# Kernel tuning notes

Hardware: AMD Instinct MI355X
Metric: run time of the kernel (lower is better)

## Reference

```python
import jax, jax.numpy as jnp
import numpy as np

B, N, D, H = 2, 2048, 1024, 16
HD = D // H  # 64
EPS = 1e-6


def setup_inputs() -> dict:
    key = jax.random.key(0)
    ks = jax.random.split(key, 16)
    rnd = lambda k, shp: jax.random.normal(k, shp, dtype=jnp.float32)
    w = lambda k, i, o: rnd(k, (i, o)) * 0.02  # stored as (in, out); y = x @ W
    return {
        "x": rnd(ks[0], (B, N, D)),
        "emb_B_D": rnd(ks[1], (B, D)),
        "gate": rnd(ks[2], (B, D)),
        "crossattn_emb": rnd(ks[3], (B, 128, D)),
        "rope_emb_L_1_1_D": rnd(ks[4], (N, HD)),
        "Wq1": w(ks[5], D, D), "Wq2": w(ks[6], D, D),
        "Wk1": w(ks[7], D, D), "Wk2": w(ks[8], D, D),
        "Wv": w(ks[9], D, D),
        "Wo": w(ks[10], D, D),
        "Wada1": w(ks[11], D, D),
        "Wada2": w(ks[12], D, 2 * D),
        "bada2": jnp.zeros((2 * D,), dtype=jnp.float32),
    }


def rotate_half(t):
    t1, t2 = jnp.split(t, 2, axis=-1)
    return jnp.concatenate([-t2, t1], axis=-1)


def reference(x, emb_B_D, gate, crossattn_emb, rope_emb_L_1_1_D,
              Wq1, Wq2, Wk1, Wk2, Wv, Wo, Wada1, Wada2, bada2):
    # adaLN modulation: SiLU -> Linear(no bias) -> Linear(bias)
    ada = jax.nn.silu(emb_B_D) @ Wada1 @ Wada2 + bada2          # [B, 2D]
    shift, scale = jnp.split(ada, 2, axis=1)                    # [B, D] each

    # LayerNorm (no affine) + scale/shift
    mu = jnp.mean(x, axis=-1, keepdims=True)
    var = jnp.var(x, axis=-1, keepdims=True)
    xn = (x - mu) * jax.lax.rsqrt(var + EPS)
    xn = xn * (1.0 + scale[:, None, :]) + shift[:, None, :]     # [B, N, D]

    # QKV projections (each to_q/to_k is two stacked linears, to_v one)
    q = xn @ Wq1 @ Wq2
    k = xn @ Wk1 @ Wk2
    v = xn @ Wv
    split_heads = lambda t: t.reshape(B, N, H, HD).transpose(0, 2, 1, 3)  # b h n d
    q, k, v = split_heads(q), split_heads(k), split_heads(v)

    # RoPE
    cos = jnp.cos(rope_emb_L_1_1_D)[None, None]                 # [1,1,N,HD]
    sin = jnp.sin(rope_emb_L_1_1_D)[None, None]
    q = q * cos + rotate_half(q) * sin
    k = k * cos + rotate_half(k) * sin

    # Attention
    sim = jnp.einsum("bhid,bhjd->bhij", q, k) * (HD ** -0.5)
    attn = jax.nn.softmax(sim, axis=-1)
    out = jnp.einsum("bhij,bhjd->bhid", attn, v)
    out = out.transpose(0, 2, 1, 3).reshape(B, N, D) @ Wo

    # Gated residual
    return x + gate[:, None, :] * out
```

## Files before the change

### kernel.cpp

```cpp
#include <hip/hip_runtime.h>
#include <stdint.h>
#include <math.h>

typedef unsigned short u16;
typedef __attribute__((ext_vector_type(8))) short short8;
typedef __attribute__((ext_vector_type(4))) float f32x4;
typedef __attribute__((ext_vector_type(4))) unsigned short u16x4;
typedef __attribute__((ext_vector_type(2))) unsigned int uint2v;

#define DEV static __device__ __forceinline__

DEV u16 f2bf(float f) {
    unsigned u = __builtin_bit_cast(unsigned, f);
    u = u + 0x7fffu + ((u >> 16) & 1u);
    return (u16)(u >> 16);
}
DEV float bf2f(u16 s) { return __builtin_bit_cast(float, ((unsigned)s) << 16); }
DEV unsigned pk2(float a, float b) {
    unsigned ua = __builtin_bit_cast(unsigned, a) + 0x8000u;
    unsigned ub = __builtin_bit_cast(unsigned, b) + 0x8000u;
    return (ua >> 16) | (ub & 0xffff0000u);
}

DEV void gl_lds16(const u16* g, u16* l) {
#if __has_builtin(__builtin_amdgcn_global_load_lds)
    __builtin_amdgcn_global_load_lds((const __attribute__((address_space(1))) unsigned int*)g,
                                     (__attribute__((address_space(3))) unsigned int*)l, 16, 0, 0);
#else
    *(short8*)l = *(const short8*)g;
#endif
}


__global__ __launch_bounds__(256) void k_ada1(const float* __restrict__ emb, const float* __restrict__ W,
                                              float* __restrict__ out) {
    int col = blockIdx.x * 64 + (threadIdx.x & 63);
    int b = blockIdx.y;
    int kseg = threadIdx.x >> 6;
    float acc = 0.f;
    for (int k = kseg * 256; k < kseg * 256 + 256; k++) {
        float e = emb[b * 1024 + k];
        float se = e / (1.f + __expf(-e));
        acc += se * W[(size_t)k * 1024 + col];
    }
    __shared__ float red[4][64];
    red[kseg][threadIdx.x & 63] = acc;
    __syncthreads();
    if (threadIdx.x < 64)
        out[b * 1024 + blockIdx.x * 64 + threadIdx.x] =
            red[0][threadIdx.x] + red[1][threadIdx.x] + red[2][threadIdx.x] + red[3][threadIdx.x];
}

__global__ __launch_bounds__(256) void k_ada2(const float* __restrict__ t, const float* __restrict__ W,
                                              const float* __restrict__ bias, float* __restrict__ out) {
    int col = blockIdx.x * 64 + (threadIdx.x & 63);
    int b = blockIdx.y;
    int kseg = threadIdx.x >> 6;
    float acc = 0.f;
    for (int k = kseg * 256; k < kseg * 256 + 256; k++)
        acc += t[b * 1024 + k] * W[(size_t)k * 2048 + col];
    __shared__ float red[4][64];
    red[kseg][threadIdx.x & 63] = acc;
    __syncthreads();
    if (threadIdx.x < 64) {
        int c = blockIdx.x * 64 + threadIdx.x;
        out[b * 2048 + c] = red[0][threadIdx.x] + red[1][threadIdx.x] +
                            red[2][threadIdx.x] + red[3][threadIdx.x] + bias[c];
    }
}

__global__ __launch_bounds__(256) void k_conv(const float* s0, u16* d0, const float* s1, u16* d1,
                                              const float* s2, u16* d2, const float* s3, u16* d3,
                                              const float* s4, u16* d4, const float* s5, u16* d5) {
    __shared__ u16 tile[64][65];
    const float* s; u16* d;
    switch (blockIdx.z) {
        case 0: s = s0; d = d0; break;
        case 1: s = s1; d = d1; break;
        case 2: s = s2; d = d2; break;
        case 3: s = s3; d = d3; break;
        case 4: s = s4; d = d4; break;
        default: s = s5; d = d5; break;
    }
    int k0 = blockIdx.x * 64, n0 = blockIdx.y * 64;
    int tx = threadIdx.x & 63, ty = threadIdx.x >> 6;
    if (blockIdx.z >= 4) {
        #pragma unroll
        for (int i = 0; i < 16; i++) {
            int kk = ty + 4 * i;
            d[(size_t)(k0 + kk) * 1024 + n0 + tx] = f2bf(s[(size_t)(k0 + kk) * 1024 + n0 + tx]);
        }
        return;
    }
    #pragma unroll
    for (int i = 0; i < 16; i++) {
        int kk = ty + 4 * i;
        tile[kk][tx] = f2bf(s[(size_t)(k0 + kk) * 1024 + n0 + tx]);
    }
    __syncthreads();
    #pragma unroll
    for (int i = 0; i < 16; i++) {
        int nn = ty + 4 * i;
        d[(size_t)(n0 + nn) * 1024 + k0 + tx] = tile[tx][nn];
    }
}

__global__ __launch_bounds__(256) void k_ln(const float* __restrict__ x, const float* __restrict__ ada,
                                            u16* __restrict__ xn, const float* __restrict__ rope,
                                            float* __restrict__ cst, float* __restrict__ snt) {
    if (blockIdx.x < 512) {
        int idx = blockIdx.x * 256 + threadIdx.x;
        float sv, cv;
        __sincosf(rope[idx], &sv, &cv);
        cst[idx] = cv; snt[idx] = sv;
    }
    int row = blockIdx.x;
    int b = row >> 11;
    float4 v = ((const float4*)(x + (size_t)row * 1024))[threadIdx.x];
    float s = v.x + v.y + v.z + v.w;
    float ss = v.x * v.x + v.y * v.y + v.z * v.z + v.w * v.w;
    #pragma unroll
    for (int m = 1; m < 64; m <<= 1) { s += __shfl_xor(s, m, 64); ss += __shfl_xor(ss, m, 64); }
    __shared__ float red[2][4];
    int wave = threadIdx.x >> 6, lane = threadIdx.x & 63;
    if (lane == 0) { red[0][wave] = s; red[1][wave] = ss; }
    __syncthreads();
    s = red[0][0] + red[0][1] + red[0][2] + red[0][3];
    ss = red[1][0] + red[1][1] + red[1][2] + red[1][3];
    float mu = s * (1.f / 1024.f);
    float var = ss * (1.f / 1024.f) - mu * mu;
    float rs = rsqrtf(var + 1e-6f);
    int c = threadIdx.x * 4;
    const float* sh = ada + b * 2048;
    const float* sc = ada + b * 2048 + 1024;
    u16x4 r;
    r.x = f2bf((v.x - mu) * rs * (1.f + sc[c + 0]) + sh[c + 0]);
    r.y = f2bf((v.y - mu) * rs * (1.f + sc[c + 1]) + sh[c + 1]);
    r.z = f2bf((v.z - mu) * rs * (1.f + sc[c + 2]) + sh[c + 2]);
    r.w = f2bf((v.w - mu) * rs * (1.f + sc[c + 3]) + sh[c + 3]);
    *(u16x4*)(xn + (size_t)row * 1024 + c) = r;
}

template <int BM, int BN, int MODE>
DEV void gemm_core(const u16* __restrict__ A, const u16* __restrict__ Bt,
                   u16* __restrict__ Cb, float* __restrict__ Cf,
                   const float* __restrict__ Xres, const float* __restrict__ gate,
                   const float* __restrict__ cst, const float* __restrict__ snt,
                   float scale, int Nn, int K, int m0, int n0) {
    constexpr int MI = BM / 32, NJ = BN / 32;
    __shared__ u16 As[BM][64];
    __shared__ u16 Bs[BN][64];
    int tid = threadIdx.x;
    int lane = tid & 63, wave = tid >> 6;
    int wm = (wave & 1) * (BM / 2), wn = (wave >> 1) * (BN / 2);
    int lr = lane & 15, quad = lane >> 4;
    f32x4 acc[MI][NJ];
    #pragma unroll
    for (int i = 0; i < MI; i++)
        #pragma unroll
        for (int j = 0; j < NJ; j++) acc[i][j] = f32x4{0.f, 0.f, 0.f, 0.f};

    int arow = tid >> 3;
    int acol = (tid & 7) * 8;
    int g8 = (((tid & 7) ^ (arow & 7))) * 8;
    int cc[2] = { ((quad ^ (lr & 7))) * 8, (((4 + quad) ^ (lr & 7))) * 8 };

    for (int k0 = 0; k0 < K; k0 += 64) {
        #pragma unroll
        for (int p = 0; p < MI; p++)
            gl_lds16(A + (size_t)(m0 + arow + 32 * p) * K + k0 + g8, &As[arow + 32 * p][acol]);
        #pragma unroll
        for (int p = 0; p < NJ; p++)
            gl_lds16(Bt + (size_t)(n0 + arow + 32 * p) * K + k0 + g8, &Bs[arow + 32 * p][acol]);
        __syncthreads();
        #pragma unroll
        for (int ks = 0; ks < 2; ks++) {
            short8 af[MI], bfr[NJ];
            #pragma unroll
            for (int i = 0; i < MI; i++) af[i] = *(const short8*)(&As[wm + i * 16 + lr][cc[ks]]);
            #pragma unroll
            for (int j = 0; j < NJ; j++) bfr[j] = *(const short8*)(&Bs[wn + j * 16 + lr][cc[ks]]);
            #pragma unroll
            for (int i = 0; i < MI; i++)
                #pragma unroll
                for (int j = 0; j < NJ; j++)
                    acc[i][j] = __builtin_amdgcn_mfma_f32_16x16x32_bf16(af[i], bfr[j], acc[i][j], 0, 0, 0);
        }
        __syncthreads();
    }

    if (MODE == 2 && (n0 + wn) < 2048) {
        #pragma unroll
        for (int i = 0; i < MI; i++)
            #pragma unroll
            for (int jp = 0; jp < 2; jp++)
                #pragma unroll
                for (int r = 0; r < 4; r++) {
                    int row = m0 + wm + i * 16 + quad * 4 + r;
                    int n = row & 2047;
                    int d1 = jp * 16 + lr;
                    float c1 = cst[n * 64 + d1],      s1 = snt[n * 64 + d1];
                    float c2 = cst[n * 64 + d1 + 32], s2 = snt[n * 64 + d1 + 32];
                    float x1 = acc[i][jp][r], x2 = acc[i][jp + 2][r];
                    Cb[(size_t)row * Nn + n0 + wn + d1]      = f2bf(x1 * c1 - x2 * s1);
                    Cb[(size_t)row * Nn + n0 + wn + d1 + 32] = f2bf(x2 * c2 + x1 * s2);
                }
        return;
    }
    #pragma unroll
    for (int i = 0; i < MI; i++)
        #pragma unroll
        for (int j = 0; j < NJ; j++)
            #pragma unroll
            for (int r = 0; r < 4; r++) {
                int row = m0 + wm + i * 16 + quad * 4 + r;
                int col = n0 + wn + j * 16 + lr;
                float v = acc[i][j][r];
                if (MODE == 1) {
                    int b = row >> 11;
                    Cf[(size_t)row * Nn + col] = Xres[(size_t)row * Nn + col] + gate[b * 1024 + col] * v;
                } else {
                    Cb[(size_t)row * Nn + col] = f2bf(v * scale);
                }
            }
}

template <int BM, int BN, int MODE>
__global__ __launch_bounds__(256) void gemm_bt(const u16* __restrict__ A, const u16* __restrict__ Bt,
                                               u16* __restrict__ Cb, float* __restrict__ Cf,
                                               const float* __restrict__ Xres, const float* __restrict__ gate,
                                               const float* __restrict__ cst, const float* __restrict__ snt,
                                               int Nn, int K) {
    gemm_core<BM, BN, MODE>(A, Bt, Cb, Cf, Xres, gate, cst, snt, 1.f, Nn, K,
                            blockIdx.y * BM, blockIdx.x * BN);
}

__global__ __launch_bounds__(256) void gemm_fold(const u16* A0, const u16* B0, u16* C0,
                                                 const u16* A1, const u16* B1, u16* C1) {
    const u16* A = blockIdx.z ? A1 : A0;
    const u16* Bt = blockIdx.z ? B1 : B0;
    u16* C = blockIdx.z ? C1 : C0;
    float scale = blockIdx.z ? 1.0f : 0.125f;
    gemm_core<64, 64, 0>(A, Bt, C, nullptr, nullptr, nullptr, nullptr, nullptr, scale,
                         1024, 1024, blockIdx.y * 64, blockIdx.x * 64);
}

__global__ __launch_bounds__(256) void k_vtrans(const u16* __restrict__ v, u16* __restrict__ vt) {
    __shared__ u16 tile[64][65];
    int n0 = blockIdx.x * 64;
    int bh = blockIdx.y; int b = bh >> 4, h = bh & 15;
    int tx = threadIdx.x & 63, ty = threadIdx.x >> 6;
    #pragma unroll
    for (int i = 0; i < 16; i++) {
        int nn = ty + 4 * i;
        tile[nn][tx] = v[(size_t)(b * 2048 + n0 + nn) * 3072 + 2048 + h * 64 + tx];
    }
    __syncthreads();
    #pragma unroll
    for (int i = 0; i < 16; i++) {
        int dd = ty + 4 * i;
        vt[((size_t)bh * 64 + dd) * 2048 + n0 + tx] = tile[tx][dd];
    }
}

__global__ __launch_bounds__(256) void k_attn(const u16* __restrict__ qkv, const u16* __restrict__ vt,
                                              float* __restrict__ paO, float* __restrict__ paL) {
    __shared__ u16 pool[128 * 72];
    __shared__ u16 Ks[2][64][64];
    __shared__ u16 Vs[2][64][64];
    int q0 = blockIdx.x * 128;
    int bh = blockIdx.y; int b = bh >> 4, h = bh & 15;
    int z = blockIdx.z;
    int kbase = z * 1024;
    int tid = threadIdx.x;
    int lane = tid & 63, wave = tid >> 6;
    int lr = lane & 15, quad = lane >> 4;
    int srow = tid >> 3, scol = (tid & 7) * 8;
    int sg = (((tid & 7) ^ (srow & 7))) * 8;
    int cc[2] = { ((quad ^ (lr & 7))) * 8, (((4 + quad) ^ (lr & 7))) * 8 };

    const u16* kp = qkv + ((size_t)(b * 2048 + kbase + srow)) * 3072 + 1024 + h * 64 + sg;
    const u16* vp = vt + ((size_t)(bh * 64 + srow)) * 2048 + kbase + sg;

    #pragma unroll
    for (int p = 0; p < 4; p++)
        gl_lds16(qkv + ((size_t)(b * 2048 + q0 + srow + 32 * p)) * 3072 + h * 64 + sg,
                 pool + (srow + 32 * p) * 64 + scol);

    short8 krA[2], vrA[2], krB[2], vrB[2];
    krA[0] = *(const short8*)(kp);               krA[1] = *(const short8*)(kp + (size_t)32 * 3072);
    vrA[0] = *(const short8*)(vp);               vrA[1] = *(const short8*)(vp + (size_t)32 * 2048);
    __syncthreads();
    short8 qf[2][2];
    #pragma unroll
    for (int rt = 0; rt < 2; rt++)
        #pragma unroll
        for (int ks = 0; ks < 2; ks++)
            qf[rt][ks] = *(const short8*)(pool + (wave * 32 + rt * 16 + lr) * 64 + cc[ks]);
    *(short8*)(&Ks[0][srow][scol])      = krA[0];
    *(short8*)(&Ks[0][srow + 32][scol]) = krA[1];
    *(short8*)(&Vs[0][srow][scol])      = vrA[0];
    *(short8*)(&Vs[0][srow + 32][scol]) = vrA[1];
    krB[0] = *(const short8*)(kp + (size_t)64 * 3072);  krB[1] = *(const short8*)(kp + (size_t)96 * 3072);
    vrB[0] = *(const short8*)(vp + 64);                 vrB[1] = *(const short8*)(vp + 64 + (size_t)32 * 2048);
    __syncthreads();

    float l_part[2] = {0.f, 0.f};
    f32x4 oacc[2][4];
    #pragma unroll
    for (int rt = 0; rt < 2; rt++)
        #pragma unroll
        for (int dt = 0; dt < 4; dt++) oacc[rt][dt] = f32x4{0.f, 0.f, 0.f, 0.f};

    auto body = [&](int it, int cur, short8 (&krF)[2], short8 (&vrF)[2],
                    short8 (&krH)[2], short8 (&vrH)[2]) {
        if (it < 14) {
            const u16* kq = kp + (size_t)(it + 2) * 64 * 3072;
            const u16* vq = vp + (it + 2) * 64;
            krF[0] = *(const short8*)(kq);  krF[1] = *(const short8*)(kq + (size_t)32 * 3072);
            vrF[0] = *(const short8*)(vq);  vrF[1] = *(const short8*)(vq + (size_t)32 * 2048);
        }
        f32x4 st[2][4];
        #pragma unroll
        for (int rt = 0; rt < 2; rt++)
            #pragma unroll
            for (int ct = 0; ct < 4; ct++) st[rt][ct] = f32x4{0.f, 0.f, 0.f, 0.f};
        #pragma unroll
        for (int ks = 0; ks < 2; ks++) {
            short8 kf[4];
            #pragma unroll
            for (int ct = 0; ct < 4; ct++)
                kf[ct] = *(const short8*)(&Ks[cur][ct * 16 + lr][cc[ks]]);
            #pragma unroll
            for (int rt = 0; rt < 2; rt++)
                #pragma unroll
                for (int ct = 0; ct < 4; ct++)
                    st[rt][ct] = __builtin_amdgcn_mfma_f32_16x16x32_bf16(kf[ct], qf[rt][ks], st[rt][ct], 0, 0, 0);
        }
        #pragma unroll
        for (int rt = 0; rt < 2; rt++)
            #pragma unroll
            for (int ct = 0; ct < 4; ct++) {
                float p0 = __expf(st[rt][ct][0]);
                float p1 = __expf(st[rt][ct][1]);
                float p2 = __expf(st[rt][ct][2]);
                float p3 = __expf(st[rt][ct][3]);
                l_part[rt] += (p0 + p1) + (p2 + p3);
                uint2v w; w.x = pk2(p0, p1); w.y = pk2(p2, p3);
                *(uint2v*)(pool + (wave * 32 + rt * 16 + lr) * 72 + ct * 16 + quad * 4) = w;
            }
        #pragma unroll
        for (int ks = 0; ks < 2; ks++) {
            short8 pf[2], vf[4];
            #pragma unroll
            for (int rt = 0; rt < 2; rt++)
                pf[rt] = *(const short8*)(pool + (wave * 32 + rt * 16 + lr) * 72 + ks * 32 + quad * 8);
            #pragma unroll
            for (int dt = 0; dt < 4; dt++)
                vf[dt] = *(const short8*)(&Vs[cur][dt * 16 + lr][cc[ks]]);
            #pragma unroll
            for (int rt = 0; rt < 2; rt++)
                #pragma unroll
                for (int dt = 0; dt < 4; dt++)
                    oacc[rt][dt] = __builtin_amdgcn_mfma_f32_16x16x32_bf16(pf[rt], vf[dt], oacc[rt][dt], 0, 0, 0);
        }
        if (it < 15) {
            int nxt = cur ^ 1;
            *(short8*)(&Ks[nxt][srow][scol])      = krH[0];
            *(short8*)(&Ks[nxt][srow + 32][scol]) = krH[1];
            *(short8*)(&Vs[nxt][srow][scol])      = vrH[0];
            *(short8*)(&Vs[nxt][srow + 32][scol]) = vrH[1];
        }
        __syncthreads();
    };

    #pragma unroll 1
    for (int it2 = 0; it2 < 8; ++it2) {
        body(2 * it2,     0, krA, vrA, krB, vrB);
        body(2 * it2 + 1, 1, krB, vrB, krA, vrA);
    }

    #pragma unroll
    for (int rt = 0; rt < 2; rt++) {
        float l = l_part[rt];
        l += __shfl_xor(l, 16, 64);
        l += __shfl_xor(l, 32, 64);
        if (quad == 0)
            paL[(size_t)z * 65536 + bh * 2048 + q0 + wave * 32 + rt * 16 + lr] = l;
    }
    float* po = paO + (size_t)z * 4096 * 1024;
    #pragma unroll
    for (int rt = 0; rt < 2; rt++)
        #pragma unroll
        for (int dt = 0; dt < 4; dt++)
            #pragma unroll
            for (int r = 0; r < 4; r++) {
                int row = q0 + wave * 32 + rt * 16 + quad * 4 + r;
                po[((size_t)(b * 2048 + row)) * 1024 + h * 64 + dt * 16 + lr] = oacc[rt][dt][r];
            }
}

__global__ __launch_bounds__(256) void k_comb(const float* __restrict__ paO, const float* __restrict__ paL,
                                              u16* __restrict__ aob) {
    int row = blockIdx.x;
    int b = row >> 11, n = row & 2047;
    int c = threadIdx.x * 4;
    int h = c >> 6;
    float l0 = paL[(b * 16 + h) * 2048 + n];
    float l1 = paL[65536 + (b * 16 + h) * 2048 + n];
    float inv = 1.f / (l0 + l1);
    float4 o0 = *(const float4*)(paO + (size_t)row * 1024 + c);
    float4 o1 = *(const float4*)(paO + (size_t)4096 * 1024 + (size_t)row * 1024 + c);
    u16x4 r;
    r.x = f2bf((o0.x + o1.x) * inv);
    r.y = f2bf((o0.y + o1.y) * inv);
    r.z = f2bf((o0.z + o1.z) * inv);
    r.w = f2bf((o0.w + o1.w) * inv);
    *(u16x4*)(aob + (size_t)row * 1024 + c) = r;
}

extern "C" void kernel_launch(void* const* d_in, const int* in_sizes, int n_in,
                              void* d_out, int out_size, void* d_ws, size_t ws_size,
                              hipStream_t stream) {
    const float* x     = (const float*)d_in[0];
    const float* emb   = (const float*)d_in[1];
    const float* gate  = (const float*)d_in[2];
    const float* rope  = (const float*)d_in[4];
    const float* Wq1   = (const float*)d_in[5];
    const float* Wq2   = (const float*)d_in[6];
    const float* Wk1   = (const float*)d_in[7];
    const float* Wk2   = (const float*)d_in[8];
    const float* Wv    = (const float*)d_in[9];
    const float* Wo    = (const float*)d_in[10];
    const float* Wada1 = (const float*)d_in[11];
    const float* Wada2 = (const float*)d_in[12];
    const float* bada2 = (const float*)d_in[13];
    float* out = (float*)d_out;

    char* ws = (char*)d_ws;
    size_t off = 0;
    auto alloc = [&](size_t bytes) { void* p = ws + off; off += (bytes + 255) & ~(size_t)255; return p; };
    float* t_ada = (float*)alloc(2048 * 4);
    float* ada   = (float*)alloc(4096 * 4);
    float* cst   = (float*)alloc((size_t)131072 * 4);
    float* snt   = (float*)alloc((size_t)131072 * 4);
    u16* xn    = (u16*)alloc((size_t)4096 * 1024 * 2);
    u16* Wq1b  = (u16*)alloc((size_t)1024 * 1024 * 2);
    u16* Wk1b  = (u16*)alloc((size_t)1024 * 1024 * 2);
    u16* Wq2t  = (u16*)alloc((size_t)1024 * 1024 * 2);
    u16* Wk2t  = (u16*)alloc((size_t)1024 * 1024 * 2);
    u16* Wot   = (u16*)alloc((size_t)1024 * 1024 * 2);
    u16* WqkvT = (u16*)alloc((size_t)3072 * 1024 * 2);
    u16* qkvb  = (u16*)alloc((size_t)4096 * 3072 * 2);
    u16* vtb   = (u16*)alloc((size_t)4096 * 1024 * 2);
    u16* aob   = (u16*)alloc((size_t)4096 * 1024 * 2);
    float* paO = (float*)alloc((size_t)2 * 4096 * 1024 * 4);
    float* paL = (float*)alloc((size_t)2 * 65536 * 4);
    (void)ws_size; (void)in_sizes; (void)n_in; (void)out_size;

    k_ada1<<<dim3(16, 2), 256, 0, stream>>>(emb, Wada1, t_ada);
    k_ada2<<<dim3(32, 2), 256, 0, stream>>>(t_ada, Wada2, bada2, ada);

    k_conv<<<dim3(16, 16, 6), 256, 0, stream>>>(Wq2, Wq2t, Wk2, Wk2t,
                                                Wv, WqkvT + (size_t)2048 * 1024, Wo, Wot,
                                                Wq1, Wq1b, Wk1, Wk1b);

    k_ln<<<4096, 256, 0, stream>>>(x, ada, xn, rope, cst, snt);

    gemm_fold<<<dim3(16, 16, 2), 256, 0, stream>>>(Wq2t, Wq1b, WqkvT,
                                                   Wk2t, Wk1b, WqkvT + (size_t)1024 * 1024);

    gemm_bt<128, 128, 2><<<dim3(24, 32), 256, 0, stream>>>(xn, WqkvT, qkvb, nullptr, nullptr, nullptr,
                                                           cst, snt, 3072, 1024);

    k_vtrans<<<dim3(32, 32), 256, 0, stream>>>(qkvb, vtb);

    k_attn<<<dim3(16, 32, 2), 256, 0, stream>>>(qkvb, vtb, paO, paL);
    k_comb<<<4096, 256, 0, stream>>>(paO, paL, aob);

    gemm_bt<128, 64, 1><<<dim3(16, 32), 256, 0, stream>>>(aob, Wot, nullptr, out, x, gate,
                                                          nullptr, nullptr, 1024, 1024);
}
```

Baseline: 306.5 us.

## Fuse prep kernels, write V transposed from QKV GEMM, bf16 attention partials

Merges the ada2 linear and the RoPE sin/cos table into the weight-conversion kernel, so k_ada2 no longer runs as its own launch and the table leaves k_ln. The QKV GEMM epilogue now writes V directly in transposed per-head layout, which removes the k_vtrans kernel and shrinks the qkv buffer to Q and K only. Attention partial outputs are stored as bf16 in a thread-local dump layout instead of fp32 rows, cutting split-combine traffic. Softmax uses hardware exp2 with log2(e) folded into the Q scale. Storing partials in bf16 loses some precision before normalization.

```diff
diff --git a/kernel.cpp b/kernel.cpp
--- a/kernel.cpp
+++ b/kernel.cpp
@@ -20,6 +20,13 @@
     unsigned ua = __builtin_bit_cast(unsigned, a) + 0x8000u;
     unsigned ub = __builtin_bit_cast(unsigned, b) + 0x8000u;
     return (ua >> 16) | (ub & 0xffff0000u);
+}
+DEV float fexp2(float x) {
+#if __has_builtin(__builtin_amdgcn_exp2f)
+    return __builtin_amdgcn_exp2f(x);
+#else
+    return __expf(x * 0.69314718056f);
+#endif
 }
 
 DEV void gl_lds16(const u16* g, u16* l) {
@@ -51,28 +58,44 @@
             red[0][threadIdx.x] + red[1][threadIdx.x] + red[2][threadIdx.x] + red[3][threadIdx.x];
 }
 
-__global__ __launch_bounds__(256) void k_ada2(const float* __restrict__ t, const float* __restrict__ W,
-                                              const float* __restrict__ bias, float* __restrict__ out) {
-    int col = blockIdx.x * 64 + (threadIdx.x & 63);
-    int b = blockIdx.y;
-    int kseg = threadIdx.x >> 6;
-    float acc = 0.f;
-    for (int k = kseg * 256; k < kseg * 256 + 256; k++)
-        acc += t[b * 1024 + k] * W[(size_t)k * 2048 + col];
+__global__ __launch_bounds__(256) void k_prep(const float* s0, u16* d0, const float* s1, u16* d1,
+                                              const float* s2, u16* d2, const float* s3, u16* d3,
+                                              const float* s4, u16* d4, const float* s5, u16* d5,
+                                              const float* __restrict__ t_ada, const float* __restrict__ Wada2,
+                                              const float* __restrict__ bada2, float* __restrict__ ada,
+                                              const float* __restrict__ rope,
+                                              float* __restrict__ cst, float* __restrict__ snt) {
+    __shared__ u16 tile[64][65];
     __shared__ float red[4][64];
-    red[kseg][threadIdx.x & 63] = acc;
-    __syncthreads();
-    if (threadIdx.x < 64) {
-        int c = blockIdx.x * 64 + threadIdx.x;
-        out[b * 2048 + c] = red[0][threadIdx.x] + red[1][threadIdx.x] +
-                            red[2][threadIdx.x] + red[3][threadIdx.x] + bias[c];
-    }
-}
-
-__global__ __launch_bounds__(256) void k_conv(const float* s0, u16* d0, const float* s1, u16* d1,
-                                              const float* s2, u16* d2, const float* s3, u16* d3,
-                                              const float* s4, u16* d4, const float* s5, u16* d5) {
-    __shared__ u16 tile[64][65];
+    if (blockIdx.z == 6) {
+        int flat = blockIdx.y * 16 + blockIdx.x;
+        if (flat < 64) {
+            int b = flat >> 5, xb = flat & 31;
+            int col = xb * 64 + (threadIdx.x & 63);
+            int kseg = threadIdx.x >> 6;
+            float acc = 0.f;
+            for (int k = kseg * 256; k < kseg * 256 + 256; k++)
+                acc += t_ada[b * 1024 + k] * Wada2[(size_t)k * 2048 + col];
+            red[kseg][threadIdx.x & 63] = acc;
+            __syncthreads();
+            if (threadIdx.x < 64) {
+                int c = xb * 64 + threadIdx.x;
+                ada[b * 2048 + c] = red[0][threadIdx.x] + red[1][threadIdx.x] +
+                                    red[2][threadIdx.x] + red[3][threadIdx.x] + bada2[c];
+            }
+        } else if (flat < 192) {
+            int idx = (flat - 64) * 1024 + threadIdx.x * 4;
+            float4 rv = *(const float4*)(rope + idx);
+            float4 cv, sv;
+            __sincosf(rv.x, &sv.x, &cv.x);
+            __sincosf(rv.y, &sv.y, &cv.y);
+            __sincosf(rv.z, &sv.z, &cv.z);
+            __sincosf(rv.w, &sv.w, &cv.w);
+            *(float4*)(cst + idx) = cv;
+            *(float4*)(snt + idx) = sv;
+        }
+        return;
+    }
     const float* s; u16* d;
     switch (blockIdx.z) {
         case 0: s = s0; d = d0; break;
@@ -106,14 +129,7 @@
 }
 
 __global__ __launch_bounds__(256) void k_ln(const float* __restrict__ x, const float* __restrict__ ada,
-                                            u16* __restrict__ xn, const float* __restrict__ rope,
-                                            float* __restrict__ cst, float* __restrict__ snt) {
-    if (blockIdx.x < 512) {
-        int idx = blockIdx.x * 256 + threadIdx.x;
-        float sv, cv;
-        __sincosf(rope[idx], &sv, &cv);
-        cst[idx] = cv; snt[idx] = sv;
-    }
+                                            u16* __restrict__ xn) {
     int row = blockIdx.x;
     int b = row >> 11;
     float4 v = ((const float4*)(x + (size_t)row * 1024))[threadIdx.x];
@@ -143,7 +159,7 @@
 
 template <int BM, int BN, int MODE>
 DEV void gemm_core(const u16* __restrict__ A, const u16* __restrict__ Bt,
-                   u16* __restrict__ Cb, float* __restrict__ Cf,
+                   u16* __restrict__ Cb, float* __restrict__ Cf, u16* __restrict__ Vt,
                    const float* __restrict__ Xres, const float* __restrict__ gate,
                    const float* __restrict__ cst, const float* __restrict__ snt,
                    float scale, int Nn, int K, int m0, int n0) {
@@ -189,22 +205,38 @@
         __syncthreads();
     }
 
-    if (MODE == 2 && (n0 + wn) < 2048) {
-        #pragma unroll
-        for (int i = 0; i < MI; i++)
-            #pragma unroll
-            for (int jp = 0; jp < 2; jp++)
+    if (MODE == 2) {
+        if ((n0 + wn) < 2048) {
+            #pragma unroll
+            for (int i = 0; i < MI; i++)
                 #pragma unroll
-                for (int r = 0; r < 4; r++) {
-                    int row = m0 + wm + i * 16 + quad * 4 + r;
-                    int n = row & 2047;
-                    int d1 = jp * 16 + lr;
-                    float c1 = cst[n * 64 + d1],      s1 = snt[n * 64 + d1];
-                    float c2 = cst[n * 64 + d1 + 32], s2 = snt[n * 64 + d1 + 32];
-                    float x1 = acc[i][jp][r], x2 = acc[i][jp + 2][r];
-                    Cb[(size_t)row * Nn + n0 + wn + d1]      = f2bf(x1 * c1 - x2 * s1);
-                    Cb[(size_t)row * Nn + n0 + wn + d1 + 32] = f2bf(x2 * c2 + x1 * s2);
+                for (int jp = 0; jp < 2; jp++)
+                    #pragma unroll
+                    for (int r = 0; r < 4; r++) {
+                        int row = m0 + wm + i * 16 + quad * 4 + r;
+                        int n = row & 2047;
+                        int d1 = jp * 16 + lr;
+                        float c1 = cst[n * 64 + d1],      s1 = snt[n * 64 + d1];
+                        float c2 = cst[n * 64 + d1 + 32], s2 = snt[n * 64 + d1 + 32];
+                        float x1 = acc[i][jp][r], x2 = acc[i][jp + 2][r];
+                        Cb[(size_t)row * Nn + n0 + wn + d1]      = f2bf(x1 * c1 - x2 * s1);
+                        Cb[(size_t)row * Nn + n0 + wn + d1 + 32] = f2bf(x2 * c2 + x1 * s2);
+                    }
+        } else {
+            int hv = (n0 + wn - 2048) >> 6;
+            #pragma unroll
+            for (int i = 0; i < MI; i++)
+                #pragma unroll
+                for (int j = 0; j < NJ; j++) {
+                    int token = m0 + wm + i * 16 + quad * 4;
+                    int bb = token >> 11;
+                    int nloc = token & 2047;
+                    u16x4 w;
+                    w.x = f2bf(acc[i][j][0]); w.y = f2bf(acc[i][j][1]);
+                    w.z = f2bf(acc[i][j][2]); w.w = f2bf(acc[i][j][3]);
+                    *(u16x4*)(Vt + ((size_t)((bb * 16 + hv) * 64 + j * 16 + lr)) * 2048 + nloc) = w;
                 }
+        }
         return;
     }
     #pragma unroll
@@ -228,10 +260,11 @@
 template <int BM, int BN, int MODE>
 __global__ __launch_bounds__(256) void gemm_bt(const u16* __restrict__ A, const u16* __restrict__ Bt,
                                                u16* __restrict__ Cb, float* __restrict__ Cf,
+                                               u16* __restrict__ Vt,
                                                const float* __restrict__ Xres, const float* __restrict__ gate,
                                                const float* __restrict__ cst, const float* __restrict__ snt,
                                                int Nn, int K) {
-    gemm_core<BM, BN, MODE>(A, Bt, Cb, Cf, Xres, gate, cst, snt, 1.f, Nn, K,
+    gemm_core<BM, BN, MODE>(A, Bt, Cb, Cf, Vt, Xres, gate, cst, snt, 1.f, Nn, K,
                             blockIdx.y * BM, blockIdx.x * BN);
 }
 
@@ -240,31 +273,13 @@
     const u16* A = blockIdx.z ? A1 : A0;
     const u16* Bt = blockIdx.z ? B1 : B0;
     u16* C = blockIdx.z ? C1 : C0;
-    float scale = blockIdx.z ? 1.0f : 0.125f;
-    gemm_core<64, 64, 0>(A, Bt, C, nullptr, nullptr, nullptr, nullptr, nullptr, scale,
+    float scale = blockIdx.z ? 1.0f : 0.18033688f;
+    gemm_core<64, 64, 0>(A, Bt, C, nullptr, nullptr, nullptr, nullptr, nullptr, nullptr, scale,
                          1024, 1024, blockIdx.y * 64, blockIdx.x * 64);
 }
 
-__global__ __launch_bounds__(256) void k_vtrans(const u16* __restrict__ v, u16* __restrict__ vt) {
-    __shared__ u16 tile[64][65];
-    int n0 = blockIdx.x * 64;
-    int bh = blockIdx.y; int b = bh >> 4, h = bh & 15;
-    int tx = threadIdx.x & 63, ty = threadIdx.x >> 6;
-    #pragma unroll
-    for (int i = 0; i < 16; i++) {
-        int nn = ty + 4 * i;
-        tile[nn][tx] = v[(size_t)(b * 2048 + n0 + nn) * 3072 + 2048 + h * 64 + tx];
-    }
-    __syncthreads();
-    #pragma unroll
-    for (int i = 0; i < 16; i++) {
-        int dd = ty + 4 * i;
-        vt[((size_t)bh * 64 + dd) * 2048 + n0 + tx] = tile[tx][dd];
-    }
-}
-
 __global__ __launch_bounds__(256) void k_attn(const u16* __restrict__ qkv, const u16* __restrict__ vt,
-                                              float* __restrict__ paO, float* __restrict__ paL) {
+                                              u16* __restrict__ dump, float* __restrict__ paL) {
     __shared__ u16 pool[128 * 72];
     __shared__ u16 Ks[2][64][64];
     __shared__ u16 Vs[2][64][64];
@@ -279,16 +294,16 @@
     int sg = (((tid & 7) ^ (srow & 7))) * 8;
     int cc[2] = { ((quad ^ (lr & 7))) * 8, (((4 + quad) ^ (lr & 7))) * 8 };
 
-    const u16* kp = qkv + ((size_t)(b * 2048 + kbase + srow)) * 3072 + 1024 + h * 64 + sg;
+    const u16* kp = qkv + ((size_t)(b * 2048 + kbase + srow)) * 2048 + 1024 + h * 64 + sg;
     const u16* vp = vt + ((size_t)(bh * 64 + srow)) * 2048 + kbase + sg;
 
     #pragma unroll
     for (int p = 0; p < 4; p++)
-        gl_lds16(qkv + ((size_t)(b * 2048 + q0 + srow + 32 * p)) * 3072 + h * 64 + sg,
+        gl_lds16(qkv + ((size_t)(b * 2048 + q0 + srow + 32 * p)) * 2048 + h * 64 + sg,
                  pool + (srow + 32 * p) * 64 + scol);
 
     short8 krA[2], vrA[2], krB[2], vrB[2];
-    krA[0] = *(const short8*)(kp);               krA[1] = *(const short8*)(kp + (size_t)32 * 3072);
+    krA[0] = *(const short8*)(kp);               krA[1] = *(const short8*)(kp + (size_t)32 * 2048);
     vrA[0] = *(const short8*)(vp);               vrA[1] = *(const short8*)(vp + (size_t)32 * 2048);
     __syncthreads();
     short8 qf[2][2];
@@ -301,7 +316,7 @@
     *(short8*)(&Ks[0][srow + 32][scol]) = krA[1];
     *(short8*)(&Vs[0][srow][scol])      = vrA[0];
     *(short8*)(&Vs[0][srow + 32][scol]) = vrA[1];
-    krB[0] = *(const short8*)(kp + (size_t)64 * 3072);  krB[1] = *(const short8*)(kp + (size_t)96 * 3072);
+    krB[0] = *(const short8*)(kp + (size_t)64 * 2048);  krB[1] = *(const short8*)(kp + (size_t)96 * 2048);
     vrB[0] = *(const short8*)(vp + 64);                 vrB[1] = *(const short8*)(vp + 64 + (size_t)32 * 2048);
     __syncthreads();
 
@@ -315,9 +330,9 @@
     auto body = [&](int it, int cur, short8 (&krF)[2], short8 (&vrF)[2],
                     short8 (&krH)[2], short8 (&vrH)[2]) {
         if (it < 14) {
-            const u16* kq = kp + (size_t)(it + 2) * 64 * 3072;
+            const u16* kq = kp + (size_t)(it + 2) * 64 * 2048;
             const u16* vq = vp + (it + 2) * 64;
-            krF[0] = *(const short8*)(kq);  krF[1] = *(const short8*)(kq + (size_t)32 * 3072);
+            krF[0] = *(const short8*)(kq);  krF[1] = *(const short8*)(kq + (size_t)32 * 2048);
             vrF[0] = *(const short8*)(vq);  vrF[1] = *(const short8*)(vq + (size_t)32 * 2048);
         }
         f32x4 st[2][4];
@@ -341,10 +356,10 @@
         for (int rt = 0; rt < 2; rt++)
             #pragma unroll
             for (int ct = 0; ct < 4; ct++) {
-                float p0 = __expf(st[rt][ct][0]);
-                float p1 = __expf(st[rt][ct][1]);
-                float p2 = __expf(st[rt][ct][2]);
-                float p3 = __expf(st[rt][ct][3]);
+                float p0 = fexp2(st[rt][ct][0]);
+                float p1 = fexp2(st[rt][ct][1]);
+                float p2 = fexp2(st[rt][ct][2]);
+                float p3 = fexp2(st[rt][ct][3]);
                 l_part[rt] += (p0 + p1) + (p2 + p3);
                 uint2v w; w.x = pk2(p0, p1); w.y = pk2(p2, p3);
                 *(uint2v*)(pool + (wave * 32 + rt * 16 + lr) * 72 + ct * 16 + quad * 4) = w;
@@ -388,35 +403,50 @@
         if (quad == 0)
             paL[(size_t)z * 65536 + bh * 2048 + q0 + wave * 32 + rt * 16 + lr] = l;
     }
-    float* po = paO + (size_t)z * 4096 * 1024;
+    u16* dp = dump + (size_t)z * 4194304 + ((size_t)(bh * 16 + blockIdx.x) * 256 + tid) * 32;
     #pragma unroll
     for (int rt = 0; rt < 2; rt++)
         #pragma unroll
-        for (int dt = 0; dt < 4; dt++)
+        for (int dt = 0; dt < 4; dt++) {
+            u16x4 w;
+            w.x = f2bf(oacc[rt][dt][0]); w.y = f2bf(oacc[rt][dt][1]);
+            w.z = f2bf(oacc[rt][dt][2]); w.w = f2bf(oacc[rt][dt][3]);
+            *(u16x4*)(dp + rt * 16 + dt * 4) = w;
+        }
+}
+
+__global__ __launch_bounds__(256) void k_comb(const u16* __restrict__ dump, const float* __restrict__ paL,
+                                              u16* __restrict__ aob) {
+    int bx = blockIdx.x, bh = blockIdx.y;
+    int b = bh >> 4, h = bh & 15;
+    int tid = threadIdx.x;
+    int lane = tid & 63, wave = tid >> 6;
+    int lr = lane & 15, quad = lane >> 4;
+    int q0 = bx * 128;
+    const u16* d0 = dump + ((size_t)(bh * 16 + bx) * 256 + tid) * 32;
+    const u16* d1 = d0 + 4194304;
+    #pragma unroll
+    for (int rt = 0; rt < 2; rt++) {
+        float inv[4];
+        #pragma unroll
+        for (int r = 0; r < 4; r++) {
+            int row = q0 + wave * 32 + rt * 16 + quad * 4 + r;
+            float l0 = paL[bh * 2048 + row];
+            float l1 = paL[65536 + bh * 2048 + row];
+            inv[r] = 1.f / (l0 + l1);
+        }
+        #pragma unroll
+        for (int dt = 0; dt < 4; dt++) {
+            u16x4 w0 = *(const u16x4*)(d0 + rt * 16 + dt * 4);
+            u16x4 w1 = *(const u16x4*)(d1 + rt * 16 + dt * 4);
             #pragma unroll
             for (int r = 0; r < 4; r++) {
                 int row = q0 + wave * 32 + rt * 16 + quad * 4 + r;
-                po[((size_t)(b * 2048 + row)) * 1024 + h * 64 + dt * 16 + lr] = oacc[rt][dt][r];
+                float o = (bf2f(((const u16*)&w0)[r]) + bf2f(((const u16*)&w1)[r])) * inv[r];
+                aob[((size_t)(b * 2048 + row)) * 1024 + h * 64 + dt * 16 + lr] = f2bf(o);
             }
-}
-
-__global__ __launch_bounds__(256) void k_comb(const float* __restrict__ paO, const float* __restrict__ paL,
-                                              u16* __restrict__ aob) {
-    int row = blockIdx.x;
-    int b = row >> 11, n = row & 2047;
-    int c = threadIdx.x * 4;
-    int h = c >> 6;
-    float l0 = paL[(b * 16 + h) * 2048 + n];
-    float l1 = paL[65536 + (b * 16 + h) * 2048 + n];
-    float inv = 1.f / (l0 + l1);
-    float4 o0 = *(const float4*)(paO + (size_t)row * 1024 + c);
-    float4 o1 = *(const float4*)(paO + (size_t)4096 * 1024 + (size_t)row * 1024 + c);
-    u16x4 r;
-    r.x = f2bf((o0.x + o1.x) * inv);
-    r.y = f2bf((o0.y + o1.y) * inv);
-    r.z = f2bf((o0.z + o1.z) * inv);
-    r.w = f2bf((o0.w + o1.w) * inv);
-    *(u16x4*)(aob + (size_t)row * 1024 + c) = r;
+        }
+    }
 }
 
 extern "C" void kernel_launch(void* const* d_in, const int* in_sizes, int n_in,
@@ -451,33 +481,31 @@
     u16* Wk2t  = (u16*)alloc((size_t)1024 * 1024 * 2);
     u16* Wot   = (u16*)alloc((size_t)1024 * 1024 * 2);
     u16* WqkvT = (u16*)alloc((size_t)3072 * 1024 * 2);
-    u16* qkvb  = (u16*)alloc((size_t)4096 * 3072 * 2);
+    u16* qkvb  = (u16*)alloc((size_t)4096 * 2048 * 2);
     u16* vtb   = (u16*)alloc((size_t)4096 * 1024 * 2);
     u16* aob   = (u16*)alloc((size_t)4096 * 1024 * 2);
-    float* paO = (float*)alloc((size_t)2 * 4096 * 1024 * 4);
+    u16* dumpO = (u16*)alloc((size_t)2 * 4194304 * 2);
     float* paL = (float*)alloc((size_t)2 * 65536 * 4);
     (void)ws_size; (void)in_sizes; (void)n_in; (void)out_size;
 
     k_ada1<<<dim3(16, 2), 256, 0, stream>>>(emb, Wada1, t_ada);
-    k_ada2<<<dim3(32, 2), 256, 0, stream>>>(t_ada, Wada2, bada2, ada);
-
-    k_conv<<<dim3(16, 16, 6), 256, 0, stream>>>(Wq2, Wq2t, Wk2, Wk2t,
+
+    k_prep<<<dim3(16, 16, 7), 256, 0, stream>>>(Wq2, Wq2t, Wk2, Wk2t,
                                                 Wv, WqkvT + (size_t)2048 * 1024, Wo, Wot,
-                                                Wq1, Wq1b, Wk1, Wk1b);
-
-    k_ln<<<4096, 256, 0, stream>>>(x, ada, xn, rope, cst, snt);
+                                                Wq1, Wq1b, Wk1, Wk1b,
+                                                t_ada, Wada2, bada2, ada, rope, cst, snt);
+
+    k_ln<<<4096, 256, 0, stream>>>(x, ada, xn);
 
     gemm_fold<<<dim3(16, 16, 2), 256, 0, stream>>>(Wq2t, Wq1b, WqkvT,
                                                    Wk2t, Wk1b, WqkvT + (size_t)1024 * 1024);
 
-    gemm_bt<128, 128, 2><<<dim3(24, 32), 256, 0, stream>>>(xn, WqkvT, qkvb, nullptr, nullptr, nullptr,
-                                                           cst, snt, 3072, 1024);
-
-    k_vtrans<<<dim3(32, 32), 256, 0, stream>>>(qkvb, vtb);
-
-    k_attn<<<dim3(16, 32, 2), 256, 0, stream>>>(qkvb, vtb, paO, paL);
-    k_comb<<<4096, 256, 0, stream>>>(paO, paL, aob);
-
-    gemm_bt<128, 64, 1><<<dim3(16, 32), 256, 0, stream>>>(aob, Wot, nullptr, out, x, gate,
+    gemm_bt<128, 128, 2><<<dim3(24, 32), 256, 0, stream>>>(xn, WqkvT, qkvb, nullptr, vtb,
+                                                           nullptr, nullptr, cst, snt, 2048, 1024);
+
+    k_attn<<<dim3(16, 32, 2), 256, 0, stream>>>(qkvb, vtb, dumpO, paL);
+    k_comb<<<dim3(16, 32), 256, 0, stream>>>(dumpO, paL, aob);
+
+    gemm_bt<128, 64, 1><<<dim3(16, 32), 256, 0, stream>>>(aob, Wot, nullptr, out, nullptr, x, gate,
                                                           nullptr, nullptr, 1024, 1024);
 }
```

Result: faster. 293.4 us (-4.3%).
